# Performance work log

Hardware: AMD Instinct MI355X
Metric: run time of the kernel (lower is better)

Reference implementation:

```python
import jax, jax.numpy as jnp
import numpy as np
import math

D_MODEL = 2048
H = 16
Q_LORA = 1536
KV_LORA = 512
DN = 128   # qk_nope_head_dim
DR = 64    # qk_rope_head_dim
DV = 128   # v_head_dim
B, S = 2, 2048
EPS = 1e-5


def layernorm(x, g, b):
    mu = jnp.mean(x, axis=-1, keepdims=True)
    var = jnp.mean(jnp.square(x - mu), axis=-1, keepdims=True)
    return (x - mu) * jax.lax.rsqrt(var + EPS) * g + b


def rope_cos_sin(position_ids, dim):
    inv_freq = 1.0 / (10000.0 ** (jnp.arange(0, dim, 2, dtype=jnp.float32) / dim))
    ang = position_ids.astype(jnp.float32)[:, None] * inv_freq[None, :]  # [S, dim/2]
    return jnp.cos(ang), jnp.sin(ang)


def apply_rope(x, cos, sin):
    # x: [..., S, ..., dim]; cos/sin broadcastable [..., S, ..., dim/2]
    x1, x2 = jnp.split(x, 2, axis=-1)
    return jnp.concatenate([x1 * cos - x2 * sin, x1 * sin + x2 * cos], axis=-1)


def setup_inputs() -> dict:
    key = jax.random.key(0)
    ks = jax.random.split(key, 8)
    sc = 0.02
    return {
        "hidden_states": jax.random.normal(ks[0], (B, S, D_MODEL), jnp.float32),
        "w_qa": jax.random.normal(ks[1], (Q_LORA, D_MODEL), jnp.float32) * sc,
        "ln_qa_g": jnp.ones((Q_LORA,), jnp.float32),
        "ln_qa_b": jnp.zeros((Q_LORA,), jnp.float32),
        "w_qb": jax.random.normal(ks[2], (H * DN, Q_LORA), jnp.float32) * sc,
        "w_qrope": jax.random.normal(ks[3], (H * DR, Q_LORA), jnp.float32) * sc,
        "w_kva": jax.random.normal(ks[4], (KV_LORA + DR, D_MODEL), jnp.float32) * sc,
        "ln_kva_g": jnp.ones((KV_LORA,), jnp.float32),
        "ln_kva_b": jnp.zeros((KV_LORA,), jnp.float32),
        "w_kvb": jax.random.normal(ks[5], (H * (DN + DV), KV_LORA), jnp.float32) * sc,
        "w_o": jax.random.normal(ks[6], (D_MODEL, H * DV), jnp.float32) * sc,
        "position_ids": jnp.arange(S, dtype=jnp.int32),
    }


def reference(hidden_states, w_qa, ln_qa_g, ln_qa_b, w_qb, w_qrope,
              w_kva, ln_kva_g, ln_kva_b, w_kvb, w_o, position_ids):
    bsz, seq_len, _ = hidden_states.shape

    # --- Q path (low-rank) ---
    q_latent = layernorm(hidden_states @ w_qa.T, ln_qa_g, ln_qa_b)        # [B,S,Q_LORA]
    q_nope = (q_latent @ w_qb.T).reshape(bsz, seq_len, H, DN)             # [B,S,H,DN]
    q_rope = (q_latent @ w_qrope.T).reshape(bsz, seq_len, H, DR)          # [B,S,H,DR]

    # --- absorb k up-projection into q ---
    k_up = w_kvb[: H * DN].reshape(H, DN, KV_LORA)
    v_up = w_kvb[H * DN:].reshape(H, DV, KV_LORA)
    q_abs = jnp.einsum('bshd,hdr->bshr', q_nope, k_up)                    # [B,S,H,R]

    # --- KV latent path ---
    kv_mixed = hidden_states @ w_kva.T                                    # [B,S,R+DR]
    kv_latent = layernorm(kv_mixed[..., :KV_LORA], ln_kva_g, ln_kva_b)    # [B,S,R]
    k_rope = kv_mixed[..., KV_LORA:]                                      # [B,S,DR]

    # --- RoPE ---
    cos, sin = rope_cos_sin(position_ids, DR)                             # [S,DR/2]
    q_rope = apply_rope(q_rope, cos[None, :, None, :], sin[None, :, None, :])
    k_rope = apply_rope(k_rope, cos[None, :, :], sin[None, :, :])

    # --- attention over latent channel (keys shared across heads) ---
    q_full = jnp.concatenate([q_abs, q_rope], axis=-1)                    # [B,S,H,R+DR]
    k_full = jnp.concatenate([kv_latent, k_rope], axis=-1)                # [B,S,R+DR]
    scale = 1.0 / math.sqrt(DN + DR)
    scores = jnp.einsum('bqhc,bkc->bhqk', q_full, k_full) * scale
    probs = jax.nn.softmax(scores, axis=-1)
    attn = jnp.einsum('bhqk,bkr->bhqr', probs, kv_latent)                 # [B,H,S,R]

    # --- absorbed v up-projection + output ---
    attn_v = jnp.einsum('bhqr,hvr->bqhv', attn, v_up)                     # [B,S,H,DV]
    attn_v = attn_v.reshape(bsz, seq_len, H * DV)
    return attn_v @ w_o.T                                                 # [B,S,D_MODEL]
```

## Files before the change

### kernel.cpp

```cpp
#include <hip/hip_runtime.h>
#include <math.h>

#define D_MODEL 2048
#define NH 16
#define Q_LORA 1536
#define KV_LORA 512
#define DN 128
#define DR 64
#define DV 128
#define BB 2
#define SS 2048
#define NROWS (BB*SS)
#define LN_EPS 1e-5f

typedef __attribute__((ext_vector_type(8))) short short8;
typedef __attribute__((ext_vector_type(4))) float f32x4;

__device__ __forceinline__ ushort f2bf(float f) {
    unsigned int u = __float_as_uint(f);
    u = u + 0x7fffu + ((u >> 16) & 1u);
    return (ushort)(u >> 16);
}

__device__ __forceinline__ float fexp2(float x) {
#if __has_builtin(__builtin_amdgcn_exp2f)
    return __builtin_amdgcn_exp2f(x);
#else
    return exp2f(x);
#endif
}

__device__ __forceinline__ void cv4(const float* __restrict__ s,
                                    ushort* __restrict__ d, long i) {
    float4 v = ((const float4*)s)[i];
    ushort4 o;
    o.x = f2bf(v.x); o.y = f2bf(v.y); o.z = f2bf(v.z); o.w = f2bf(v.w);
    ((ushort4*)d)[i] = o;
}

__global__ __launch_bounds__(256)
void cvt_all(const float* __restrict__ hs,     const float* __restrict__ w_qa,
             const float* __restrict__ w_qb,   const float* __restrict__ w_qrope,
             const float* __restrict__ w_kvb,  const float* __restrict__ w_kva,
             ushort* __restrict__ hs_bf,       ushort* __restrict__ w_qa_bf,
             ushort* __restrict__ w_qb_bf,     ushort* __restrict__ w_qrope_bf,
             ushort* __restrict__ w_kvb_bf,    ushort* __restrict__ w_kva_bf,
             const int* __restrict__ pos,      float2* __restrict__ tab)
{
    long i = (long)blockIdx.x * 256 + threadIdx.x;
    if (i < 2097152) { cv4(hs, hs_bf, i); return; }
    i -= 2097152;
    if (i < 786432) { cv4(w_qa, w_qa_bf, i); return; }
    i -= 786432;
    if (i < 786432) { cv4(w_qb, w_qb_bf, i); return; }
    i -= 786432;
    if (i < 393216) { cv4(w_qrope, w_qrope_bf, i); return; }
    i -= 393216;
    if (i < 524288) { cv4(w_kvb, w_kvb_bf, i); return; }
    i -= 524288;
    if (i < 327680) {
        long e = i * 4;
        int row = (int)(e >> 11), col = (int)(e & 2047);
        ushort4 o;
        if (row < 576) {
            float4 v = *(const float4*)(w_kva + (long)row * 2048 + col);
            o.x = f2bf(v.x); o.y = f2bf(v.y); o.z = f2bf(v.z); o.w = f2bf(v.w);
        } else { o.x = 0; o.y = 0; o.z = 0; o.w = 0; }
        *(ushort4*)(w_kva_bf + (long)row * 2048 + col) = o;
        return;
    }
    i -= 327680;
    if (i >= 65536) return;
    int idx = (int)i;
    int fi = idx & 31;
    int s = idx >> 5;
    double ang = (double)pos[s] * exp(-(double)fi * 0.28782313662425572);
    float2 cs;
    cs.x = (float)cos(ang);
    cs.y = (float)sin(ang);
    tab[idx] = cs;
}

#define GLL16(g, l) \
    __builtin_amdgcn_global_load_lds((const __attribute__((address_space(1))) void*)(g), \
                                     (__attribute__((address_space(3))) void*)(l), 16, 0, 0)

__device__ __forceinline__ void gemm_core32(const ushort* __restrict__ A,
    const ushort* __restrict__ Bp, ushort* As, ushort* Bs,
    int K, int lda, int ldb, int m0, int n0, int tid, f32x4 acc[4][4])
{
    int l = tid & 63, w = tid >> 6;
    int l15 = l & 15, quad = l >> 4;
    int wm = (w >> 1) * 64, wn = (w & 1) * 64;
    int ob = tid * 16;
    int row = ob >> 6, colb = ob & 63;
    const char* ga0 = (const char*)(A  + (long)(m0 + row) * lda)      + colb;
    const char* ga1 = (const char*)(A  + (long)(m0 + row + 64) * lda) + colb;
    const char* gb0 = (const char*)(Bp + (long)(n0 + row) * ldb)      + colb;
    const char* gb1 = (const char*)(Bp + (long)(n0 + row + 64) * ldb) + colb;
    ushort* la0 = As + tid * 8;
    ushort* la1 = As + 2048 + tid * 8;
    ushort* lb0 = Bs + tid * 8;
    ushort* lb1 = Bs + 2048 + tid * 8;

    for (int k0 = 0; k0 < K; k0 += 32) {
        GLL16(ga0, la0); GLL16(ga1, la1);
        GLL16(gb0, lb0); GLL16(gb1, lb1);
        ga0 += 64; ga1 += 64; gb0 += 64; gb1 += 64;
        __syncthreads();
        short8 af[4], bf[4];
        #pragma unroll
        for (int i = 0; i < 4; ++i)
            af[i] = *(const short8*)(As + (wm + i * 16 + l15) * 32 + quad * 8);
        #pragma unroll
        for (int j = 0; j < 4; ++j)
            bf[j] = *(const short8*)(Bs + (wn + j * 16 + l15) * 32 + quad * 8);
        #pragma unroll
        for (int i = 0; i < 4; ++i)
            #pragma unroll
            for (int j = 0; j < 4; ++j)
                acc[i][j] = __builtin_amdgcn_mfma_f32_16x16x32_bf16(
                    af[i], bf[j], acc[i][j], 0, 0, 0);
        __syncthreads();
    }
}

__device__ __forceinline__ void gemm_core64(const ushort* __restrict__ A,
    const ushort* __restrict__ Bp, ushort* As, ushort* Bs,
    int K, int lda, int ldb, int m0, int n0, int tid, f32x4 acc[4][4])
{
    int l = tid & 63, w = tid >> 6;
    int l15 = l & 15, quad = l >> 4;
    int wm = (w >> 1) * 64, wn = (w & 1) * 64;
    int row = tid >> 3;
    int cg  = ((tid & 7) ^ (row & 7)) * 8;
    const char* ga0 = (const char*)(A  + (long)(m0 + row) * lda + cg);
    const char* ga1 = (const char*)(A  + (long)(m0 + row + 32) * lda + cg);
    const char* ga2 = (const char*)(A  + (long)(m0 + row + 64) * lda + cg);
    const char* ga3 = (const char*)(A  + (long)(m0 + row + 96) * lda + cg);
    const char* gb0 = (const char*)(Bp + (long)(n0 + row) * ldb + cg);
    const char* gb1 = (const char*)(Bp + (long)(n0 + row + 32) * ldb + cg);
    const char* gb2 = (const char*)(Bp + (long)(n0 + row + 64) * ldb + cg);
    const char* gb3 = (const char*)(Bp + (long)(n0 + row + 96) * ldb + cg);
    ushort* la0 = As + tid * 8;
    ushort* la1 = As + 2048 + tid * 8;
    ushort* la2 = As + 4096 + tid * 8;
    ushort* la3 = As + 6144 + tid * 8;
    ushort* lb0 = Bs + tid * 8;
    ushort* lb1 = Bs + 2048 + tid * 8;
    ushort* lb2 = Bs + 4096 + tid * 8;
    ushort* lb3 = Bs + 6144 + tid * 8;

    for (int k0 = 0; k0 < K; k0 += 64) {
        GLL16(ga0, la0); GLL16(ga1, la1); GLL16(ga2, la2); GLL16(ga3, la3);
        GLL16(gb0, lb0); GLL16(gb1, lb1); GLL16(gb2, lb2); GLL16(gb3, lb3);
        ga0 += 128; ga1 += 128; ga2 += 128; ga3 += 128;
        gb0 += 128; gb1 += 128; gb2 += 128; gb3 += 128;
        __syncthreads();
        #pragma unroll
        for (int half = 0; half < 2; ++half) {
            short8 af[4], bf[4];
            #pragma unroll
            for (int i = 0; i < 4; ++i) {
                int r = wm + i * 16 + l15;
                af[i] = *(const short8*)(As + r * 64 + ((half * 4 + quad) ^ (l15 & 7)) * 8);
            }
            #pragma unroll
            for (int j = 0; j < 4; ++j) {
                int r = wn + j * 16 + l15;
                bf[j] = *(const short8*)(Bs + r * 64 + ((half * 4 + quad) ^ (l15 & 7)) * 8);
            }
            #pragma unroll
            for (int i = 0; i < 4; ++i)
                #pragma unroll
                for (int j = 0; j < 4; ++j)
                    acc[i][j] = __builtin_amdgcn_mfma_f32_16x16x32_bf16(
                        af[i], bf[j], acc[i][j], 0, 0, 0);
        }
        __syncthreads();
    }
}

__global__ __launch_bounds__(256, 4)
void gemm_f32out(const ushort* __restrict__ A, const ushort* __restrict__ B,
                 float* __restrict__ C, int K, int lda, int ldb, int ldc)
{
    __shared__ __align__(16) ushort As[128 * 64];
    __shared__ __align__(16) ushort Bs[128 * 64];
    int tid = threadIdx.x;
    int m0 = blockIdx.y * 128, n0 = blockIdx.x * 128;
    f32x4 acc[4][4] = {};
    gemm_core64(A, B, As, Bs, K, lda, ldb, m0, n0, tid, acc);
    int l = tid & 63, w = tid >> 6;
    int l15 = l & 15, quad = l >> 4;
    int wm = (w >> 1) * 64, wn = (w & 1) * 64;
    #pragma unroll
    for (int i = 0; i < 4; ++i)
        #pragma unroll
        for (int j = 0; j < 4; ++j)
            #pragma unroll
            for (int r = 0; r < 4; ++r) {
                long gm = m0 + wm + i * 16 + quad * 4 + r;
                long gn = n0 + wn + j * 16 + l15;
                C[gm * ldc + gn] = acc[i][j][r];
            }
}

__global__ __launch_bounds__(256, 4)
void gemm_dual(const ushort* __restrict__ A, const ushort* __restrict__ Bqa,
               const ushort* __restrict__ Bkva, float* __restrict__ Cq,
               float* __restrict__ Ckv)
{
    __shared__ __align__(16) ushort As[128 * 64];
    __shared__ __align__(16) ushort Bs[128 * 64];
    int tid = threadIdx.x;
    int bx = blockIdx.x;
    int m0 = blockIdx.y * 128;
    const ushort* Bp; float* C; int ldc, n0;
    if (bx < 12) { n0 = bx * 128;        Bp = Bqa  + (long)n0 * 2048; C = Cq;  ldc = 1536; }
    else         { n0 = (bx - 12) * 128; Bp = Bkva + (long)n0 * 2048; C = Ckv; ldc = 640; }
    f32x4 acc[4][4] = {};
    gemm_core64(A, Bp, As, Bs, D_MODEL, D_MODEL, D_MODEL, m0, 0, tid, acc);
    int l = tid & 63, w = tid >> 6;
    int l15 = l & 15, quad = l >> 4;
    int wm = (w >> 1) * 64, wn = (w & 1) * 64;
    #pragma unroll
    for (int i = 0; i < 4; ++i)
        #pragma unroll
        for (int j = 0; j < 4; ++j)
            #pragma unroll
            for (int r = 0; r < 4; ++r) {
                long gm = m0 + wm + i * 16 + quad * 4 + r;
                long gn = n0 + wn + j * 16 + l15;
                C[gm * ldc + gn] = acc[i][j][r];
            }
}

__global__ __launch_bounds__(256, 4)
void gemm_qkv(const ushort* __restrict__ Aq, const ushort* __restrict__ Bqb,
              const ushort* __restrict__ Bqr, ushort* __restrict__ qfull,
              const float2* __restrict__ tab,
              const ushort* __restrict__ Akv, const ushort* __restrict__ Bkvb,
              ushort* __restrict__ kfull, ushort* __restrict__ vt)
{
    __shared__ __align__(16) ushort As[128 * 32];
    __shared__ __align__(16) ushort Bs[128 * 32];
    int tid = threadIdx.x;
    int bx = blockIdx.x;
    int m0 = blockIdx.y * 128;
    int l = tid & 63, w = tid >> 6;
    int l15 = l & 15, quad = l >> 4;
    int wm = (w >> 1) * 64, wn = (w & 1) * 64;
    f32x4 acc[4][4] = {};

    if (bx < 24) {
        int n0 = bx * 128;
        const ushort* Bp = (n0 < 2048) ? Bqb + (long)n0 * Q_LORA
                                       : Bqr + (long)(n0 - 2048) * Q_LORA;
        gemm_core32(Aq, Bp, As, Bs, Q_LORA, Q_LORA, Q_LORA, m0, 0, tid, acc);
        if (n0 < 2048) {
            int head = n0 >> 7;
            #pragma unroll
            for (int i = 0; i < 4; ++i)
                #pragma unroll
                for (int j = 0; j < 4; ++j)
                    #pragma unroll
                    for (int r = 0; r < 4; ++r) {
                        long gm = m0 + wm + i * 16 + quad * 4 + r;
                        int c = wn + j * 16 + l15;
                        qfull[(gm * NH + head) * 192 + c] = f2bf(acc[i][j][r]);
                    }
        } else {
            int nb = n0 - 2048;
            int head = (nb + wn) >> 6;
            #pragma unroll
            for (int i = 0; i < 4; ++i)
                #pragma unroll
                for (int j = 0; j < 2; ++j)
                    #pragma unroll
                    for (int r = 0; r < 4; ++r) {
                        long gm = m0 + wm + i * 16 + quad * 4 + r;
                        int ir = j * 16 + l15;
                        int s = (int)(gm & (SS - 1));
                        float2 cs = tab[s * 32 + ir];
                        float x1 = acc[i][j][r], x2 = acc[i][j + 2][r];
                        ushort* op = qfull + (gm * NH + head) * 192 + 128;
                        op[ir]      = f2bf(x1 * cs.x - x2 * cs.y);
                        op[ir + 32] = f2bf(x1 * cs.y + x2 * cs.x);
                    }
        }
    } else {
        int n0 = (bx - 24) * 128;
        const ushort* Bp = Bkvb + (long)n0 * KV_LORA;
        gemm_core32(Akv, Bp, As, Bs, KV_LORA, KV_LORA, KV_LORA, m0, 0, tid, acc);
        if (n0 < 2048) {
            int head = n0 >> 7;
            #pragma unroll
            for (int i = 0; i < 4; ++i)
                #pragma unroll
                for (int j = 0; j < 4; ++j)
                    #pragma unroll
                    for (int r = 0; r < 4; ++r) {
                        long gm = m0 + wm + i * 16 + quad * 4 + r;
                        int c = wn + j * 16 + l15;
                        kfull[(gm * NH + head) * 192 + c] = f2bf(acc[i][j][r]);
                    }
        } else {
            int head = (n0 >> 7) - 16;
            #pragma unroll
            for (int i = 0; i < 4; ++i)
                #pragma unroll
                for (int j = 0; j < 4; ++j) {
                    long gm0 = m0 + wm + i * 16 + quad * 4;
                    int c = wn + j * 16 + l15;
                    ushort4 p;
                    p.x = f2bf(acc[i][j][0]); p.y = f2bf(acc[i][j][1]);
                    p.z = f2bf(acc[i][j][2]); p.w = f2bf(acc[i][j][3]);
                    *(ushort4*)(vt + (long)head * 128 * 4096 + (long)c * 4096 + gm0) = p;
                }
        }
    }
}

__global__ __launch_bounds__(256)
void ln_rope(const float* __restrict__ qlf, ushort* __restrict__ qlbf,
             const float* __restrict__ gqa, const float* __restrict__ bqa,
             const float* __restrict__ kvm, ushort* __restrict__ kvbf,
             const float* __restrict__ gkv, const float* __restrict__ bkv,
             ushort* __restrict__ kfull, const float2* __restrict__ tab,
             const float* __restrict__ w_o, ushort* __restrict__ w_o_bf)
{
    __shared__ float sred[4], ssred[4];
    int bid = blockIdx.x, tid = threadIdx.x;
    if (bid < 2 * NROWS) {
        const float* x; ushort* y; const float* g; const float* b; int n;
        if (bid < NROWS) {
            x = qlf + (long)bid * Q_LORA; y = qlbf + (long)bid * Q_LORA;
            g = gqa; b = bqa; n = Q_LORA;
        } else {
            int r = bid - NROWS;
            x = kvm + (long)r * 640; y = kvbf + (long)r * KV_LORA;
            g = gkv; b = bkv; n = KV_LORA;
        }
        float s = 0.f, ss = 0.f;
        for (int i = tid; i < n; i += 256) { float v = x[i]; s += v; ss += v * v; }
        #pragma unroll
        for (int off = 32; off > 0; off >>= 1) {
            s  += __shfl_xor(s, off);
            ss += __shfl_xor(ss, off);
        }
        int wid = tid >> 6, lane = tid & 63;
        if (lane == 0) { sred[wid] = s; ssred[wid] = ss; }
        __syncthreads();
        s  = sred[0] + sred[1] + sred[2] + sred[3];
        ss = ssred[0] + ssred[1] + ssred[2] + ssred[3];
        float mu  = s / n;
        float var = ss / n - mu * mu;
        float r = 1.0f / sqrtf(var + LN_EPS);
        for (int i = tid; i < n; i += 256)
            y[i] = f2bf((x[i] - mu) * r * g[i] + b[i]);
        return;
    }
    if (bid < 2 * NROWS + 512) {
        long idx = (long)(bid - 2 * NROWS) * 256 + tid;
        if (idx >= (long)NROWS * 32) return;
        int i = (int)(idx & 31);
        long rowi = idx >> 5;
        int s = (int)(rowi & (SS - 1));
        float2 cs = tab[s * 32 + i];
        float c = cs.x, sn = cs.y;
        const float* p = kvm + rowi * 640 + 512;
        float x1 = p[i], x2 = p[i + 32];
        ushort v1 = f2bf(x1 * c - x2 * sn);
        ushort v2 = f2bf(x1 * sn + x2 * c);
        ushort* o = kfull + rowi * NH * 192 + 128;
        #pragma unroll
        for (int h = 0; h < NH; ++h) {
            o[h * 192 + i]      = v1;
            o[h * 192 + i + 32] = v2;
        }
        return;
    }
    long i = (long)(bid - (2 * NROWS + 512)) * 256 + tid;
    if (i < 1048576) cv4(w_o, w_o_bf, i);
}

#define C2LOG 0.10412700456539414f
#define THR2  11.541560327111707f

__global__ __launch_bounds__(512, 4)
void flash_mfma(const ushort* __restrict__ qf, const ushort* __restrict__ kf,
                const ushort* __restrict__ vt, ushort* __restrict__ attnv)
{
    __shared__ __align__(16) ushort Ks[64 * 192];
    __shared__ __align__(16) ushort Vs[128 * 64];
    __shared__ __align__(16) ushort Ps[128 * 72];
    int tid = threadIdx.x;
    int w = tid >> 6, l = tid & 63, l15 = l & 15, quad = l >> 4;
    int bh = blockIdx.x;
    int b = bh >> 4, h = bh & 15;
    int q0 = blockIdx.y * 128;

    const ushort* qp = qf + ((long)(b * SS + q0 + 16 * w + l15) * NH + h) * 192 + quad * 8;
    short8 aq[6];
    #pragma unroll
    for (int kk = 0; kk < 6; ++kk) aq[kk] = *(const short8*)(qp + kk * 32);

    f32x4 o[8] = {};
    float lsum = 0.f;
    float mrow = -INFINITY;

    const ushort* kbase = kf + ((long)(b * SS) * NH + h) * 192;
    const ushort* vbase = vt + (long)h * 128 * 4096 + (long)b * SS;

    int r0k = tid >> 3, subk = tid & 7;
    int v0  = tid >> 2, subv = tid & 3;
    const ushort* kgp = kbase + (long)r0k * (NH * 192);
    const ushort* vgp = vbase + (long)v0 * 4096;

    short8 pk[3], pv[2];
    #pragma unroll
    for (int it = 0; it < 3; ++it)
        pk[it] = *(const short8*)(kgp + (subk + 8 * it) * 8);
    #pragma unroll
    for (int it = 0; it < 2; ++it)
        pv[it] = *(const short8*)(vgp + (subv + 4 * it) * 8);

    int ksw = r0k & 7, vsw = v0 & 7;

    for (int k0 = 0; k0 < SS; k0 += 64) {
        __syncthreads();
        #pragma unroll
        for (int it = 0; it < 3; ++it)
            *(short8*)&Ks[r0k * 192 + ((subk + 8 * it) ^ ksw) * 8] = pk[it];
        #pragma unroll
        for (int it = 0; it < 2; ++it)
            *(short8*)&Vs[v0 * 64 + ((subv + 4 * it) ^ vsw) * 8] = pv[it];
        __syncthreads();
        if (k0 + 64 < SS) {
            const ushort* kg = kgp + (long)(k0 + 64) * (NH * 192);
            const ushort* vg = vgp + (k0 + 64);
            #pragma unroll
            for (int it = 0; it < 3; ++it)
                pk[it] = *(const short8*)(kg + (subk + 8 * it) * 8);
            #pragma unroll
            for (int it = 0; it < 2; ++it)
                pv[it] = *(const short8*)(vg + (subv + 4 * it) * 8);
        }

        f32x4 sc[4] = {};
        __builtin_amdgcn_s_setprio(1);
        #pragma unroll
        for (int kk = 0; kk < 6; ++kk) {
            #pragma unroll
            for (int j = 0; j < 4; ++j) {
                int krow = j * 16 + l15;
                short8 kfr = *(const short8*)&Ks[krow * 192 + (((kk * 4 + quad) ^ (krow & 7))) * 8];
                sc[j] = __builtin_amdgcn_mfma_f32_16x16x32_bf16(kfr, aq[kk], sc[j], 0, 0, 0);
            }
        }
        __builtin_amdgcn_s_setprio(0);

        float rmax = fmaxf(
            fmaxf(fmaxf(fmaxf(sc[0][0], sc[0][1]), fmaxf(sc[0][2], sc[0][3])),
                  fmaxf(fmaxf(sc[1][0], sc[1][1]), fmaxf(sc[1][2], sc[1][3]))),
            fmaxf(fmaxf(fmaxf(sc[2][0], sc[2][1]), fmaxf(sc[2][2], sc[2][3])),
                  fmaxf(fmaxf(sc[3][0], sc[3][1]), fmaxf(sc[3][2], sc[3][3]))));
        rmax = fmaxf(rmax, __shfl_xor(rmax, 16));
        rmax = fmaxf(rmax, __shfl_xor(rmax, 32));
        float pmax = rmax * C2LOG;

        if (__any(pmax > mrow + THR2)) {
            float mnew = fmaxf(mrow, pmax);
            float alpha = fexp2(mrow - mnew);
            mrow = mnew;
            lsum *= alpha;
            float a0 = __shfl(alpha, quad * 4 + 0);
            float a1 = __shfl(alpha, quad * 4 + 1);
            float a2 = __shfl(alpha, quad * 4 + 2);
            float a3 = __shfl(alpha, quad * 4 + 3);
            #pragma unroll
            for (int v8 = 0; v8 < 8; ++v8) {
                o[v8][0] *= a0; o[v8][1] *= a1;
                o[v8][2] *= a2; o[v8][3] *= a3;
            }
        }

        float tsum = 0.f;
        int prow = (16 * w + l15) * 72 + quad * 4;
        #pragma unroll
        for (int j = 0; j < 4; ++j) {
            float p0 = fexp2(fmaf(sc[j][0], C2LOG, -mrow));
            float p1 = fexp2(fmaf(sc[j][1], C2LOG, -mrow));
            float p2 = fexp2(fmaf(sc[j][2], C2LOG, -mrow));
            float p3 = fexp2(fmaf(sc[j][3], C2LOG, -mrow));
            tsum += (p0 + p1) + (p2 + p3);
            uint2 pu;
            pu.x = (uint)f2bf(p0) | ((uint)f2bf(p1) << 16);
            pu.y = (uint)f2bf(p2) | ((uint)f2bf(p3) << 16);
            *(uint2*)&Ps[prow + j * 16] = pu;
        }
        tsum += __shfl_xor(tsum, 16);
        tsum += __shfl_xor(tsum, 32);
        lsum += tsum;

        __builtin_amdgcn_s_setprio(1);
        #pragma unroll
        for (int ks = 0; ks < 2; ++ks) {
            short8 pa = *(const short8*)&Ps[(16 * w + l15) * 72 + ks * 32 + quad * 8];
            #pragma unroll
            for (int v8 = 0; v8 < 8; ++v8) {
                int vrow = v8 * 16 + l15;
                short8 bv = *(const short8*)&Vs[vrow * 64 + (((ks * 4 + quad) ^ (vrow & 7))) * 8];
                o[v8] = __builtin_amdgcn_mfma_f32_16x16x32_bf16(pa, bv, o[v8], 0, 0, 0);
            }
        }
        __builtin_amdgcn_s_setprio(0);
    }

    #pragma unroll
    for (int r = 0; r < 4; ++r) {
        float Lq = __shfl(lsum, quad * 4 + r);
        float inv = 1.0f / Lq;
        long rowi = (long)(b * SS) + q0 + 16 * w + quad * 4 + r;
        ushort* op = attnv + (rowi * NH + h) * 128;
        #pragma unroll
        for (int v8 = 0; v8 < 8; ++v8)
            op[v8 * 16 + l15] = f2bf(o[v8][r] * inv);
    }
}


extern "C" void kernel_launch(void* const* d_in, const int* in_sizes, int n_in,
                              void* d_out, int out_size, void* d_ws, size_t ws_size,
                              hipStream_t stream) {
    const float* hs       = (const float*)d_in[0];
    const float* w_qa     = (const float*)d_in[1];
    const float* ln_qa_g  = (const float*)d_in[2];
    const float* ln_qa_b  = (const float*)d_in[3];
    const float* w_qb     = (const float*)d_in[4];
    const float* w_qrope  = (const float*)d_in[5];
    const float* w_kva    = (const float*)d_in[6];
    const float* ln_kva_g = (const float*)d_in[7];
    const float* ln_kva_b = (const float*)d_in[8];
    const float* w_kvb    = (const float*)d_in[9];
    const float* w_o      = (const float*)d_in[10];
    const int*   pos      = (const int*)d_in[11];
    float* out = (float*)d_out;

    char* W = (char*)d_ws;
    ushort* hs_bf     = (ushort*)(W + 0);
    ushort* w_o_bf    = (ushort*)(W + 0);
    ushort* w_qa_bf   = (ushort*)(W + 16777216);
    ushort* w_qb_bf   = (ushort*)(W + 23068672);
    ushort* w_qrope_bf= (ushort*)(W + 29360128);
    ushort* w_kva_bf  = (ushort*)(W + 32505856);
    ushort* w_kvb_bf  = (ushort*)(W + 35127296);
    float*  q_lat_f   = (float*)(W + 39321600);
    ushort* q_lat_bf  = (ushort*)(W + 64487424);
    float*  kv_mix    = (float*)(W + 77070336);
    ushort* kv_lat_bf = (ushort*)(W + 87556096);
    ushort* q_full    = (ushort*)(W + 91750400);
    ushort* k_full    = (ushort*)(W + 116916224);
    ushort* v_exp_t   = (ushort*)(W + 142082048);
    ushort* attnv_bf  = (ushort*)(W + 158859264);
    float2* rope_tab  = (float2*)(W + 158859264);

    dim3 blk(256);

    cvt_all<<<dim3(19456), blk, 0, stream>>>(
        hs, w_qa, w_qb, w_qrope, w_kvb, w_kva,
        hs_bf, w_qa_bf, w_qb_bf, w_qrope_bf, w_kvb_bf, w_kva_bf,
        pos, rope_tab);
    gemm_dual<<<dim3(17, 32), blk, 0, stream>>>(
        hs_bf, w_qa_bf, w_kva_bf, q_lat_f, kv_mix);
    ln_rope<<<dim3(12800), blk, 0, stream>>>(
        q_lat_f, q_lat_bf, ln_qa_g, ln_qa_b,
        kv_mix, kv_lat_bf, ln_kva_g, ln_kva_b,
        k_full, rope_tab, w_o, w_o_bf);
    gemm_qkv<<<dim3(56, 32), blk, 0, stream>>>(
        q_lat_bf, w_qb_bf, w_qrope_bf, q_full, rope_tab,
        kv_lat_bf, w_kvb_bf, k_full, v_exp_t);
    flash_mfma<<<dim3(BB * NH, SS / 128), dim3(512), 0, stream>>>(
        q_full, k_full, v_exp_t, attnv_bf);
    gemm_f32out<<<dim3(16, 32), blk, 0, stream>>>(
        attnv_bf, w_o_bf, out, NH * DV, NH * DV, NH * DV, D_MODEL);
}
```

Measured before the change: 450.1 us.

## Double-buffer LDS tiles in GEMM cores to overlap global loads with MFMA

Converts both GEMM inner loops to a two-stage software pipeline. The next K-tile is loaded directly into a second LDS buffer while MFMAs consume the current one, with explicit vmcnt waits and raw s_barrier plus sched_barrier in place of __syncthreads. LDS use doubles, so launch bounds for the 64-wide kernels drop from 4 to 2 blocks per CU, trading occupancy for latency hiding.

```diff
diff --git a/kernel.cpp b/kernel.cpp
--- a/kernel.cpp
+++ b/kernel.cpp
@@ -102,26 +102,41 @@
     ushort* la1 = As + 2048 + tid * 8;
     ushort* lb0 = Bs + tid * 8;
     ushort* lb1 = Bs + 2048 + tid * 8;
-
-    for (int k0 = 0; k0 < K; k0 += 32) {
-        GLL16(ga0, la0); GLL16(ga1, la1);
-        GLL16(gb0, lb0); GLL16(gb1, lb1);
-        ga0 += 64; ga1 += 64; gb0 += 64; gb1 += 64;
-        __syncthreads();
+    int NT = K >> 5;
+
+    GLL16(ga0, la0); GLL16(ga1, la1);
+    GLL16(gb0, lb0); GLL16(gb1, lb1);
+    ga0 += 64; ga1 += 64; gb0 += 64; gb1 += 64;
+
+    for (int t = 0; t < NT; ++t) {
+        int cur = (t & 1) * 4096, nxt = 4096 - cur;
+        if (t + 1 < NT) {
+            GLL16(ga0, la0 + nxt); GLL16(ga1, la1 + nxt);
+            GLL16(gb0, lb0 + nxt); GLL16(gb1, lb1 + nxt);
+            ga0 += 64; ga1 += 64; gb0 += 64; gb1 += 64;
+            asm volatile("s_waitcnt vmcnt(4)" ::: "memory");
+        } else {
+            asm volatile("s_waitcnt vmcnt(0)" ::: "memory");
+        }
+        __builtin_amdgcn_s_barrier();
+        __builtin_amdgcn_sched_barrier(0);
+        const ushort* Ac = As + cur;
+        const ushort* Bc = Bs + cur;
         short8 af[4], bf[4];
         #pragma unroll
         for (int i = 0; i < 4; ++i)
-            af[i] = *(const short8*)(As + (wm + i * 16 + l15) * 32 + quad * 8);
+            af[i] = *(const short8*)(Ac + (wm + i * 16 + l15) * 32 + quad * 8);
         #pragma unroll
         for (int j = 0; j < 4; ++j)
-            bf[j] = *(const short8*)(Bs + (wn + j * 16 + l15) * 32 + quad * 8);
+            bf[j] = *(const short8*)(Bc + (wn + j * 16 + l15) * 32 + quad * 8);
         #pragma unroll
         for (int i = 0; i < 4; ++i)
             #pragma unroll
             for (int j = 0; j < 4; ++j)
                 acc[i][j] = __builtin_amdgcn_mfma_f32_16x16x32_bf16(
                     af[i], bf[j], acc[i][j], 0, 0, 0);
-        __syncthreads();
+        __builtin_amdgcn_sched_barrier(0);
+        __builtin_amdgcn_s_barrier();
     }
 }
 
@@ -150,25 +165,42 @@
     ushort* lb1 = Bs + 2048 + tid * 8;
     ushort* lb2 = Bs + 4096 + tid * 8;
     ushort* lb3 = Bs + 6144 + tid * 8;
-
-    for (int k0 = 0; k0 < K; k0 += 64) {
-        GLL16(ga0, la0); GLL16(ga1, la1); GLL16(ga2, la2); GLL16(ga3, la3);
-        GLL16(gb0, lb0); GLL16(gb1, lb1); GLL16(gb2, lb2); GLL16(gb3, lb3);
-        ga0 += 128; ga1 += 128; ga2 += 128; ga3 += 128;
-        gb0 += 128; gb1 += 128; gb2 += 128; gb3 += 128;
-        __syncthreads();
+    int NT = K >> 6;
+
+    GLL16(ga0, la0); GLL16(ga1, la1); GLL16(ga2, la2); GLL16(ga3, la3);
+    GLL16(gb0, lb0); GLL16(gb1, lb1); GLL16(gb2, lb2); GLL16(gb3, lb3);
+    ga0 += 128; ga1 += 128; ga2 += 128; ga3 += 128;
+    gb0 += 128; gb1 += 128; gb2 += 128; gb3 += 128;
+
+    for (int t = 0; t < NT; ++t) {
+        int cur = (t & 1) * 8192, nxt = 8192 - cur;
+        if (t + 1 < NT) {
+            GLL16(ga0, la0 + nxt); GLL16(ga1, la1 + nxt);
+            GLL16(ga2, la2 + nxt); GLL16(ga3, la3 + nxt);
+            GLL16(gb0, lb0 + nxt); GLL16(gb1, lb1 + nxt);
+            GLL16(gb2, lb2 + nxt); GLL16(gb3, lb3 + nxt);
+            ga0 += 128; ga1 += 128; ga2 += 128; ga3 += 128;
+            gb0 += 128; gb1 += 128; gb2 += 128; gb3 += 128;
+            asm volatile("s_waitcnt vmcnt(8)" ::: "memory");
+        } else {
+            asm volatile("s_waitcnt vmcnt(0)" ::: "memory");
+        }
+        __builtin_amdgcn_s_barrier();
+        __builtin_amdgcn_sched_barrier(0);
+        const ushort* Ac = As + cur;
+        const ushort* Bc = Bs + cur;
         #pragma unroll
         for (int half = 0; half < 2; ++half) {
             short8 af[4], bf[4];
             #pragma unroll
             for (int i = 0; i < 4; ++i) {
                 int r = wm + i * 16 + l15;
-                af[i] = *(const short8*)(As + r * 64 + ((half * 4 + quad) ^ (l15 & 7)) * 8);
+                af[i] = *(const short8*)(Ac + r * 64 + ((half * 4 + quad) ^ (l15 & 7)) * 8);
             }
             #pragma unroll
             for (int j = 0; j < 4; ++j) {
                 int r = wn + j * 16 + l15;
-                bf[j] = *(const short8*)(Bs + r * 64 + ((half * 4 + quad) ^ (l15 & 7)) * 8);
+                bf[j] = *(const short8*)(Bc + r * 64 + ((half * 4 + quad) ^ (l15 & 7)) * 8);
             }
             #pragma unroll
             for (int i = 0; i < 4; ++i)
@@ -177,16 +209,17 @@
                     acc[i][j] = __builtin_amdgcn_mfma_f32_16x16x32_bf16(
                         af[i], bf[j], acc[i][j], 0, 0, 0);
         }
-        __syncthreads();
-    }
-}
-
-__global__ __launch_bounds__(256, 4)
+        __builtin_amdgcn_sched_barrier(0);
+        __builtin_amdgcn_s_barrier();
+    }
+}
+
+__global__ __launch_bounds__(256, 2)
 void gemm_f32out(const ushort* __restrict__ A, const ushort* __restrict__ B,
                  float* __restrict__ C, int K, int lda, int ldb, int ldc)
 {
-    __shared__ __align__(16) ushort As[128 * 64];
-    __shared__ __align__(16) ushort Bs[128 * 64];
+    __shared__ __align__(16) ushort As[2 * 128 * 64];
+    __shared__ __align__(16) ushort Bs[2 * 128 * 64];
     int tid = threadIdx.x;
     int m0 = blockIdx.y * 128, n0 = blockIdx.x * 128;
     f32x4 acc[4][4] = {};
@@ -206,13 +239,13 @@
             }
 }
 
-__global__ __launch_bounds__(256, 4)
+__global__ __launch_bounds__(256, 2)
 void gemm_dual(const ushort* __restrict__ A, const ushort* __restrict__ Bqa,
                const ushort* __restrict__ Bkva, float* __restrict__ Cq,
                float* __restrict__ Ckv)
 {
-    __shared__ __align__(16) ushort As[128 * 64];
-    __shared__ __align__(16) ushort Bs[128 * 64];
+    __shared__ __align__(16) ushort As[2 * 128 * 64];
+    __shared__ __align__(16) ushort Bs[2 * 128 * 64];
     int tid = threadIdx.x;
     int bx = blockIdx.x;
     int m0 = blockIdx.y * 128;
@@ -243,8 +276,8 @@
               const ushort* __restrict__ Akv, const ushort* __restrict__ Bkvb,
               ushort* __restrict__ kfull, ushort* __restrict__ vt)
 {
-    __shared__ __align__(16) ushort As[128 * 32];
-    __shared__ __align__(16) ushort Bs[128 * 32];
+    __shared__ __align__(16) ushort As[2 * 128 * 32];
+    __shared__ __align__(16) ushort Bs[2 * 128 * 32];
     int tid = threadIdx.x;
     int bx = blockIdx.x;
     int m0 = blockIdx.y * 128;
```

Measured after the change: 455.6 us. Within noise of the previous version (+1.2%).
